# Kernel tuning notes

Measured on AMD Instinct MI355X. Metric: run time of the kernel, lower is better.

## Reference

```python
import jax, jax.numpy as jnp
import numpy as np

H = 128  # per-direction hidden size; bidirectional output = 256


def sru_layer(x, W, b):
    """One bidirectional SRU layer (use_selu=1).
    x: (L, B, n_in); W: (n_in, 2H*k); b: (4H,) = [f-bias(2H), r-bias(2H)].
    """
    L, B, n_in = x.shape
    k = W.shape[1] // (2 * H)  # 4 if n_in != 2H else 3
    U = (x @ W).reshape(L, B, 2, H, k)  # (L,B,dir,H,k)
    bf = b[: 2 * H].reshape(2, H)
    br = b[2 * H :].reshape(2, H)
    # highway input: learned projection (k==4) or the input itself split per direction
    xp = U[..., 3] if k == 4 else x.reshape(L, B, 2, H)
    # time-reverse the backward direction so a single scan serves both
    Us = jnp.stack([U[:, :, 0, :, :3], U[::-1, :, 1, :, :3]], axis=2)  # (L,B,2,H,3)
    xps = jnp.stack([xp[:, :, 0], xp[::-1, :, 1]], axis=2)  # (L,B,2,H)

    def step(c, t):
        u, xpt = t
        xt = u[..., 0]
        f = jax.nn.sigmoid(u[..., 1] + bf)
        r = jax.nn.sigmoid(u[..., 2] + br)
        c = f * c + (1.0 - f) * xt
        h = r * jax.nn.selu(c) + (1.0 - r) * xpt
        return c, h

    c0 = jnp.zeros((B, 2, H), x.dtype)
    _, hs = jax.lax.scan(step, c0, (Us, xps))  # hs: (L,B,2,H)
    # un-reverse backward direction, concat directions -> (L,B,2H)
    return jnp.concatenate([hs[:, :, 0], hs[::-1, :, 1]], axis=-1)


def setup_inputs() -> dict:
    key = jax.random.key(0)
    ks = jax.random.split(key, 6)
    L, B, D = 1024, 64, 128
    inp = {
        "input": jax.random.normal(ks[0], (L, B, D), jnp.float32),
        "W0": jax.random.normal(ks[1], (D, 4 * 2 * H), jnp.float32) / np.sqrt(D),
        "b0": jnp.zeros((4 * H,), jnp.float32),
        "gamma": jnp.ones((2 * H,), jnp.float32),
        "beta": jnp.zeros((2 * H,), jnp.float32),
    }
    for i, kk in zip((1, 2, 3), ks[2:5]):
        inp[f"W{i}"] = jax.random.normal(kk, (2 * H, 3 * 2 * H), jnp.float32) / np.sqrt(2 * H)
        inp[f"b{i}"] = jnp.zeros((4 * H,), jnp.float32)
    return inp


def reference(input, W0, b0, W1, b1, W2, b2, W3, b3, gamma, beta):
    x = sru_layer(input, W0, b0)
    x = sru_layer(x, W1, b1)
    x = sru_layer(x, W2, b2)
    x = sru_layer(x, W3, b3)  # (L,B,256)
    # permute(1,2,0) + avg_pool1d over full length + squeeze == mean over time
    feats = jnp.mean(x, axis=0)  # (B,256)
    mu = jnp.mean(feats, axis=-1, keepdims=True)
    var = jnp.mean(jnp.square(feats - mu), axis=-1, keepdims=True)
    return (feats - mu) / jnp.sqrt(var + 1e-5) * gamma + beta
```

## Files before the change

kernel.cpp:

```cpp
#include <hip/hip_runtime.h>
#include <math.h>

#define HID 128
#define LSEQ 1024
#define NB 64
#define SUB 32
#define NQG (LSEQ / SUB)
#define NCH 16384

typedef __attribute__((ext_vector_type(4))) float f32x4;
typedef __attribute__((ext_vector_type(8))) short bf16x8;
typedef __attribute__((ext_vector_type(8))) unsigned short u16x8;
typedef __attribute__((ext_vector_type(4))) unsigned short u16x4;

#define VMCNT0() asm volatile("s_waitcnt vmcnt(0)" ::: "memory")
#define VMCNT8() asm volatile("s_waitcnt vmcnt(8)" ::: "memory")
#define LGKMCNT0() asm volatile("s_waitcnt lgkmcnt(0)" ::: "memory")

__device__ __forceinline__ unsigned short f2bf(float x) {
    union { float f; unsigned int u; } a; a.f = x;
    unsigned int r = a.u + 0x7FFFu + ((a.u >> 16) & 1u);
    return (unsigned short)(r >> 16);
}
__device__ __forceinline__ float bf2f(unsigned short h) {
    union { float f; unsigned int u; } a; a.u = ((unsigned int)h) << 16;
    return a.f;
}
__device__ __forceinline__ float sigmoidf_(float x) { return 1.0f / (1.0f + __expf(-x)); }
__device__ __forceinline__ float seluf_(float x) {
    const float sc = 1.0507009873554805f, al = 1.6732632423543772f;
    return x > 0.0f ? sc * x : sc * al * (__expf(x) - 1.0f);
}

__device__ __forceinline__ void gload16(const unsigned short* g, unsigned short* l) {
    __builtin_amdgcn_global_load_lds(
        (const __attribute__((address_space(1))) unsigned int*)g,
        (__attribute__((address_space(3))) unsigned int*)l, 16, 0, 0);
}

__global__ __launch_bounds__(256) void conv_wt(const float* __restrict__ W,
                                               unsigned short* __restrict__ Wt,
                                               int K, int N, int kw) {
    int idx = blockIdx.x * 256 + threadIdx.x;
    if (idx >= K * N) return;
    int k = idx / N, n = idx - k * N;
    const int dir = n / (128 * kw);
    const int rem = n - dir * 128 * kw;
    const int h = rem / kw, j = rem - h * kw;
    const int np = dir * 128 * kw + j * 128 + h;
    Wt[(size_t)np * K + k] = f2bf(W[idx]);
}

__global__ __launch_bounds__(256) void conv_in(const float* __restrict__ in,
                                               unsigned short* __restrict__ outp,
                                               int n4) {
    int idx = blockIdx.x * 256 + threadIdx.x;
    if (idx >= n4) return;
    const float4 v = *reinterpret_cast<const float4*>(in + (size_t)idx * 4);
    u16x4 w;
    w[0] = f2bf(v.x); w[1] = f2bf(v.y); w[2] = f2bf(v.z); w[3] = f2bf(v.w);
    *(u16x4*)(outp + (size_t)idx * 4) = w;
}

template <int K, int NC>
__global__ __launch_bounds__(256) void gemm_v4(const unsigned short* __restrict__ A,
                                               const unsigned short* __restrict__ Bt,
                                               unsigned short* __restrict__ C) {
    constexpr int NN = NC / 128;
    constexpr int NT = K / 64;
    __shared__ __align__(16) unsigned short smA[2][128 * 64];
    __shared__ __align__(16) unsigned short smB[2][128 * 64];

    const int bid = blockIdx.x;
    const int mi = bid & 7;
    const int tt = bid >> 3;
    const int n = tt % NN;
    const int mg = tt / NN;
    const int m0 = (mg * 8 + mi) * 128;
    const int n0 = n * 128;

    const int tid = threadIdx.x;
    const int r = tid >> 3, c8 = tid & 7;
    const int swz = (c8 * 8) ^ ((r & 7) * 8);

    const int lane = tid & 63;
    const int wid = tid >> 6;
    const int wr = wid >> 1, wc = wid & 1;
    const int rlo = lane & 15, g = lane >> 4;

    f32x4 acc[4][4] = {};

    const unsigned short* gA = A + (size_t)m0 * K + swz;
    const unsigned short* gB = Bt + (size_t)n0 * K + swz;

#pragma unroll
    for (int i = 0; i < 4; ++i) {
        gload16(gA + (size_t)(r + 32 * i) * K, &smA[0][i * 2048 + tid * 8]);
        gload16(gB + (size_t)(r + 32 * i) * K, &smB[0][i * 2048 + tid * 8]);
    }
    if (NT > 1) {
#pragma unroll
        for (int i = 0; i < 4; ++i) {
            gload16(gA + (size_t)(r + 32 * i) * K + 64, &smA[1][i * 2048 + tid * 8]);
            gload16(gB + (size_t)(r + 32 * i) * K + 64, &smB[1][i * 2048 + tid * 8]);
        }
        VMCNT8();
    } else {
        VMCNT0();
    }
    __builtin_amdgcn_sched_barrier(0);
    __builtin_amdgcn_s_barrier();

#pragma unroll
    for (int t = 0; t < NT; ++t) {
        const int cur = t & 1;
        bf16x8 af[2][4], bff[2][4];
#pragma unroll
        for (int kk = 0; kk < 2; ++kk) {
            const int ke = kk * 32 + g * 8;
#pragma unroll
            for (int m = 0; m < 4; ++m) {
                const int row = wr * 64 + m * 16 + rlo;
                af[kk][m] = *(const bf16x8*)(&smA[cur][row * 64 + (ke ^ ((row & 7) * 8))]);
            }
#pragma unroll
            for (int nn2 = 0; nn2 < 4; ++nn2) {
                const int row = wc * 64 + nn2 * 16 + rlo;
                bff[kk][nn2] = *(const bf16x8*)(&smB[cur][row * 64 + (ke ^ ((row & 7) * 8))]);
            }
        }
        LGKMCNT0();
        __builtin_amdgcn_sched_barrier(0);
        __builtin_amdgcn_s_barrier();
        if (t + 2 < NT) {
            const int k0 = (t + 2) * 64;
#pragma unroll
            for (int i = 0; i < 4; ++i) {
                gload16(gA + (size_t)(r + 32 * i) * K + k0, &smA[cur][i * 2048 + tid * 8]);
                gload16(gB + (size_t)(r + 32 * i) * K + k0, &smB[cur][i * 2048 + tid * 8]);
            }
        }
        __builtin_amdgcn_sched_barrier(0);
#pragma unroll
        for (int kk = 0; kk < 2; ++kk)
#pragma unroll
            for (int m = 0; m < 4; ++m)
#pragma unroll
                for (int nn2 = 0; nn2 < 4; ++nn2)
                    acc[m][nn2] = __builtin_amdgcn_mfma_f32_16x16x32_bf16(
                        af[kk][m], bff[kk][nn2], acc[m][nn2], 0, 0, 0);
        if (t + 1 < NT) {
            if (t + 2 < NT) { VMCNT8(); } else { VMCNT0(); }
            __builtin_amdgcn_sched_barrier(0);
            __builtin_amdgcn_s_barrier();
        }
    }
    __syncthreads();

    unsigned short* ep = &smA[0][0];
#pragma unroll
    for (int m = 0; m < 4; ++m)
#pragma unroll
        for (int nn2 = 0; nn2 < 4; ++nn2) {
            const int col = wc * 64 + nn2 * 16 + rlo;
#pragma unroll
            for (int j = 0; j < 4; ++j) {
                const int row = wr * 64 + m * 16 + g * 4 + j;
                const int chunk = (col >> 3) ^ (row & 15);
                ep[row * 128 + chunk * 8 + (col & 7)] = f2bf(acc[m][nn2][j]);
            }
        }
    __syncthreads();
    {
        const int rr = tid >> 1;
        const int cb = (tid & 1) * 8;
#pragma unroll
        for (int k2 = 0; k2 < 8; ++k2) {
            const int c = cb + k2;
            const int pc = c ^ (rr & 15);
            const u16x8 v = *(const u16x8*)(&ep[rr * 128 + pc * 8]);
            *(u16x8*)(&C[(size_t)(m0 + rr) * NC + n0 + c * 8]) = v;
        }
    }
}


template <int NC>
__global__ __launch_bounds__(256) void scanA(const unsigned short* __restrict__ U,
                                             const float* __restrict__ bias,
                                             float* __restrict__ aArr,
                                             float* __restrict__ bArr,
                                             int dirbase, int dbstride,
                                             int chmask, int chshift, int T) {
    const int gid = blockIdx.x * 256 + threadIdx.x;
    const int fc = gid & chmask;
    const int q = gid >> chshift;
    const int dir = dirbase + (fc >> 13);
    const int b = (fc >> 7) & 63, h = fc & 127;
    const int dbase = (fc >> 13) * dbstride;
    const float bfb = bias[dir * HID + h];

    float aa = 1.0f, cc = 0.0f;
#pragma unroll 4
    for (int i = 0; i < SUB; ++i) {
        const int s = q * SUB + i;
        const int t = dir ? (T - 1 - s) : s;
        const size_t m = (size_t)t * NB + b;
        const float u0 = bf2f(U[m * NC + dbase + h]);
        const float u1 = bf2f(U[m * NC + dbase + 128 + h]);
        const float f = sigmoidf_(u1 + bfb);
        cc = f * cc + (1.0f - f) * u0;
        aa *= f;
    }
    const int fcg = dir * 8192 + (fc & 8191);
    aArr[(size_t)q * NCH + fcg] = aa;
    bArr[(size_t)q * NCH + fcg] = cc;
}

template <int Q>
__global__ __launch_bounds__(256) void scanB(const float* __restrict__ aArr,
                                             const float* __restrict__ bArr,
                                             float* __restrict__ cin,
                                             float* __restrict__ carry,
                                             int init, int fcg0) {
    const int fcg = fcg0 + blockIdx.x * 256 + threadIdx.x;
    float a[Q], bb[Q];
#pragma unroll
    for (int q = 0; q < Q; ++q) {
        a[q]  = aArr[(size_t)q * NCH + fcg];
        bb[q] = bArr[(size_t)q * NCH + fcg];
    }
    float c = init ? 0.0f : carry[fcg];
#pragma unroll
    for (int q = 0; q < Q; ++q) {
        cin[(size_t)q * NCH + fcg] = c;
        c = a[q] * c + bb[q];
    }
    carry[fcg] = c;
}

template <int NC, bool XP_FROM_U, bool ACC>
__global__ __launch_bounds__(256) void scanC(const unsigned short* __restrict__ U,
                                             const unsigned short* __restrict__ Xprev,
                                             const float* __restrict__ bias,
                                             const float* __restrict__ cin,
                                             unsigned short* __restrict__ Xout,
                                             float* __restrict__ part,
                                             int dirbase, int dbstride,
                                             int chmask, int chshift,
                                             int T, int t0, int qg0) {
    const int gid = blockIdx.x * 256 + threadIdx.x;
    const int fc = gid & chmask;
    const int q = gid >> chshift;
    const int dir = dirbase + (fc >> 13);
    const int b = (fc >> 7) & 63, h = fc & 127;
    const int dbase = (fc >> 13) * dbstride;
    const float bfb = bias[dir * HID + h];
    const float brb = bias[2 * HID + dir * HID + h];
    const int fcg = dir * 8192 + (fc & 8191);

    float c = cin[(size_t)q * NCH + fcg];
    float psum = 0.0f;
#pragma unroll 4
    for (int i = 0; i < SUB; ++i) {
        const int s = q * SUB + i;
        const int t = dir ? (T - 1 - s) : s;
        const size_t m = (size_t)t * NB + b;
        const size_t xrow = ((size_t)(t0 + t) * NB + b) * (2 * HID) + dir * HID + h;
        const float u0 = bf2f(U[m * NC + dbase + h]);
        const float u1 = bf2f(U[m * NC + dbase + 128 + h]);
        const float u2 = bf2f(U[m * NC + dbase + 256 + h]);
        float xp;
        if constexpr (XP_FROM_U) xp = bf2f(U[m * NC + dbase + 384 + h]);
        else                     xp = bf2f(Xprev[xrow]);
        const float f = sigmoidf_(u1 + bfb);
        const float r = sigmoidf_(u2 + brb);
        c = f * c + (1.0f - f) * u0;
        const float ho = r * seluf_(c) + (1.0f - r) * xp;
        if constexpr (ACC) psum += ho;
        else               Xout[xrow] = f2bf(ho);
    }
    if constexpr (ACC)
        part[(size_t)(qg0 + q) * (NB * 256) + b * 256 + dir * HID + h] = psum;
}

__global__ __launch_bounds__(256) void pool2(const float* __restrict__ part,
                                             const float* __restrict__ gamma,
                                             const float* __restrict__ beta,
                                             float* __restrict__ out) {
    const int b = blockIdx.x, chn = threadIdx.x;
    float s = 0.0f;
#pragma unroll
    for (int i = 0; i < NQG; ++i) s += part[(size_t)i * (NB * 256) + b * 256 + chn];
    const float feat = s * (1.0f / LSEQ);
    __shared__ float red[256];
    red[chn] = feat; __syncthreads();
    for (int off = 128; off > 0; off >>= 1) { if (chn < off) red[chn] += red[chn + off]; __syncthreads(); }
    const float mu = red[0] * (1.0f / 256.0f);
    __syncthreads();
    const float d = feat - mu;
    red[chn] = d * d; __syncthreads();
    for (int off = 128; off > 0; off >>= 1) { if (chn < off) red[chn] += red[chn + off]; __syncthreads(); }
    const float var = red[0] * (1.0f / 256.0f);
    out[b * 256 + chn] = d * rsqrtf(var + 1e-5f) * gamma[chn] + beta[chn];
}

extern "C" void kernel_launch(void* const* d_in, const int* in_sizes, int n_in,
                              void* d_out, int out_size, void* d_ws, size_t ws_size,
                              hipStream_t stream) {
    const float* input = (const float*)d_in[0];
    const float* gamma = (const float*)d_in[3];
    const float* beta  = (const float*)d_in[4];
    const float* Wl[4] = { (const float*)d_in[1], (const float*)d_in[5],
                           (const float*)d_in[7], (const float*)d_in[9] };
    const float* bl[4] = { (const float*)d_in[2], (const float*)d_in[6],
                           (const float*)d_in[8], (const float*)d_in[10] };
    float* out = (float*)d_out;

    char* base = (char*)d_ws;
    size_t off = 0;
    auto alloc = [&](size_t bytes) { size_t o = off; off = (off + bytes + 255) & ~(size_t)255; return o; };

    unsigned short* Wt[4];
    Wt[0] = (unsigned short*)(base + alloc((size_t)1024 * 128 * 2));
    for (int i = 1; i < 4; ++i) Wt[i] = (unsigned short*)(base + alloc((size_t)768 * 256 * 2));
    unsigned short* Xa = (unsigned short*)(base + alloc((size_t)LSEQ * NB * 256 * 2));
    unsigned short* Xb = (unsigned short*)(base + alloc((size_t)LSEQ * NB * 256 * 2));
    unsigned short* Xc = (unsigned short*)(base + alloc((size_t)LSEQ * NB * 128 * 2));
    float* carry = (float*)(base + alloc((size_t)NCH * 4));
    float* aArr  = (float*)(base + alloc((size_t)32 * NCH * 4));
    float* bArr  = (float*)(base + alloc((size_t)32 * NCH * 4));
    float* cinArr= (float*)(base + alloc((size_t)32 * NCH * 4));
    float* part  = (float*)(base + alloc((size_t)NQG * NB * 256 * 4));
    if (ws_size < off + (1u << 21)) return;
    const size_t uavail = ws_size - off;
    unsigned short* U = (unsigned short*)(base + off);

    conv_in<<<(LSEQ * NB * 128 / 4 + 255) / 256, 256, 0, stream>>>(input, Xc, LSEQ * NB * 128 / 4);
    conv_wt<<<(128 * 1024 + 255) / 256, 256, 0, stream>>>(Wl[0], Wt[0], 128, 1024, 4);
    for (int i = 1; i < 4; ++i)
        conv_wt<<<(256 * 768 + 255) / 256, 256, 0, stream>>>(Wl[i], Wt[i], 256, 768, 3);

    const unsigned short* Xin[4] = { Xc, Xa, Xb, Xa };
    unsigned short* Xout[4] = { Xa, Xb, Xa, nullptr };

    if (uavail >= (size_t)LSEQ * NB * 1024 * 2) {
        const int T = LSEQ, Q = T / SUB;
        const int nm = T * NB / 128;
        const dim3 sgrid(NCH * Q / 256);
        for (int layer = 0; layer < 4; ++layer) {
            const int kw = (layer == 0) ? 4 : 3;
            const int dbstride = 128 * kw;
            if (layer == 0)
                gemm_v4<128, 1024><<<dim3(nm * 8), 256, 0, stream>>>(Xin[0], Wt[0], U);
            else
                gemm_v4<256, 768><<<dim3(nm * 6), 256, 0, stream>>>(Xin[layer], Wt[layer], U);
            if (layer == 0)
                scanA<1024><<<sgrid, 256, 0, stream>>>(U, bl[0], aArr, bArr, 0, dbstride,
                                                       NCH - 1, 14, T);
            else
                scanA<768><<<sgrid, 256, 0, stream>>>(U, bl[layer], aArr, bArr, 0, dbstride,
                                                      NCH - 1, 14, T);
            scanB<32><<<NCH / 256, 256, 0, stream>>>(aArr, bArr, cinArr, carry, 1, 0);
            if (layer == 0)
                scanC<1024, true, false><<<sgrid, 256, 0, stream>>>(
                    U, nullptr, bl[0], cinArr, Xout[0], nullptr, 0, dbstride, NCH - 1, 14, T, 0, 0);
            else if (layer < 3)
                scanC<768, false, false><<<sgrid, 256, 0, stream>>>(
                    U, Xin[layer], bl[layer], cinArr, Xout[layer], nullptr, 0, dbstride,
                    NCH - 1, 14, T, 0, 0);
            else
                scanC<768, false, true><<<sgrid, 256, 0, stream>>>(
                    U, Xin[3], bl[3], cinArr, nullptr, part, 0, dbstride, NCH - 1, 14, T, 0, 0);
        }
    } else {
        int T = 0;
        for (int t = 512; t >= SUB; t >>= 1)
            if ((size_t)t * NB * 512 * 2 <= uavail) { T = t; break; }
        if (T == 0) return;
        const int C = LSEQ / T, Q = T / SUB;
        const int nm = T * NB / 128;
        const dim3 sgrid(8192 * Q / 256);
        for (int layer = 0; layer < 4; ++layer) {
            const int kw = (layer == 0) ? 4 : 3;
            const int K = (layer == 0) ? 128 : 256;
            const int Nc = 128 * kw;
            for (int dir = 0; dir < 2; ++dir) {
                const unsigned short* Bts = Wt[layer] + (size_t)dir * Nc * K;
                for (int cc = 0; cc < C; ++cc) {
                    const int ci = dir ? (C - 1 - cc) : cc;
                    const unsigned short* Ap = Xin[layer] + (size_t)ci * T * NB * K;
                    if (layer == 0)
                        gemm_v4<128, 512><<<dim3(nm * 4), 256, 0, stream>>>(Ap, Bts, U);
                    else
                        gemm_v4<256, 384><<<dim3(nm * 3), 256, 0, stream>>>(Ap, Bts, U);
                    if (layer == 0)
                        scanA<512><<<sgrid, 256, 0, stream>>>(U, bl[0], aArr, bArr, dir, 0,
                                                              8191, 13, T);
                    else
                        scanA<384><<<sgrid, 256, 0, stream>>>(U, bl[layer], aArr, bArr, dir, 0,
                                                              8191, 13, T);
                    if (Q == 16)
                        scanB<16><<<32, 256, 0, stream>>>(aArr, bArr, cinArr, carry,
                                                          cc == 0 ? 1 : 0, dir * 8192);
                    else
                        scanB<32><<<32, 256, 0, stream>>>(aArr, bArr, cinArr, carry,
                                                          cc == 0 ? 1 : 0, dir * 8192);
                    if (layer == 0)
                        scanC<512, true, false><<<sgrid, 256, 0, stream>>>(
                            U, nullptr, bl[0], cinArr, Xout[0], nullptr, dir, 0,
                            8191, 13, T, ci * T, ci * Q);
                    else if (layer < 3)
                        scanC<384, false, false><<<sgrid, 256, 0, stream>>>(
                            U, Xin[layer], bl[layer], cinArr, Xout[layer], nullptr, dir, 0,
                            8191, 13, T, ci * T, ci * Q);
                    else
                        scanC<384, false, true><<<sgrid, 256, 0, stream>>>(
                            U, Xin[3], bl[3], cinArr, nullptr, part, dir, 0,
                            8191, 13, T, ci * T, ci * Q);
                }
            }
        }
    }
    pool2<<<NB, 256, 0, stream>>>(part, gamma, beta, out);
}
```

Baseline: 489.2 us.

## Restructure GEMM to keep B tile resident and stream A per-wave

Replaces the 128x128 double-buffered GEMM with one where each block holds the full-K B tile (128 columns) in LDS and loops over four 128-row M tiles. Each wave streams its own 32-row A slices through a 4-slot ring with 3-deep prefetch, so the loop needs no block-wide barriers. The LDS epilogue is dropped in favour of direct u16x4 global stores. The aim is to reuse B across more rows and cut synchronisation, at the cost of narrower, less coalesced output stores, more LDS per block, and fewer blocks in the grid.

```diff
diff --git a/kernel.cpp b/kernel.cpp
--- a/kernel.cpp
+++ b/kernel.cpp
@@ -13,9 +13,10 @@
 typedef __attribute__((ext_vector_type(8))) unsigned short u16x8;
 typedef __attribute__((ext_vector_type(4))) unsigned short u16x4;
 
-#define VMCNT0() asm volatile("s_waitcnt vmcnt(0)" ::: "memory")
-#define VMCNT8() asm volatile("s_waitcnt vmcnt(8)" ::: "memory")
-#define LGKMCNT0() asm volatile("s_waitcnt lgkmcnt(0)" ::: "memory")
+template <int N>
+__device__ __forceinline__ void vmcntN() {
+    asm volatile("s_waitcnt vmcnt(%0)" :: "n"(N) : "memory");
+}
 
 __device__ __forceinline__ unsigned short f2bf(float x) {
     union { float f; unsigned int u; } a; a.f = x;
@@ -63,127 +64,104 @@
 }
 
 template <int K, int NC>
-__global__ __launch_bounds__(256) void gemm_v4(const unsigned short* __restrict__ A,
+__global__ __launch_bounds__(256) void gemm_v5(const unsigned short* __restrict__ A,
                                                const unsigned short* __restrict__ Bt,
                                                unsigned short* __restrict__ C) {
     constexpr int NN = NC / 128;
     constexpr int NT = K / 64;
-    __shared__ __align__(16) unsigned short smA[2][128 * 64];
-    __shared__ __align__(16) unsigned short smB[2][128 * 64];
+    constexpr int NSTEP = 4 * NT;
+    __shared__ __align__(16) unsigned short smB[NT * 128 * 64];
+    __shared__ __align__(16) unsigned short smA[4][4][2048];
 
     const int bid = blockIdx.x;
     const int mi = bid & 7;
     const int tt = bid >> 3;
     const int n = tt % NN;
-    const int mg = tt / NN;
-    const int m0 = (mg * 8 + mi) * 128;
+    const int mg = (tt / NN) * 8 + mi;
+    const int mb = mg * 512;
     const int n0 = n * 128;
 
     const int tid = threadIdx.x;
-    const int r = tid >> 3, c8 = tid & 7;
-    const int swz = (c8 * 8) ^ ((r & 7) * 8);
-
-    const int lane = tid & 63;
-    const int wid = tid >> 6;
-    const int wr = wid >> 1, wc = wid & 1;
-    const int rlo = lane & 15, g = lane >> 4;
-
-    f32x4 acc[4][4] = {};
-
-    const unsigned short* gA = A + (size_t)m0 * K + swz;
-    const unsigned short* gB = Bt + (size_t)n0 * K + swz;
-
-#pragma unroll
-    for (int i = 0; i < 4; ++i) {
-        gload16(gA + (size_t)(r + 32 * i) * K, &smA[0][i * 2048 + tid * 8]);
-        gload16(gB + (size_t)(r + 32 * i) * K, &smB[0][i * 2048 + tid * 8]);
-    }
-    if (NT > 1) {
-#pragma unroll
-        for (int i = 0; i < 4; ++i) {
-            gload16(gA + (size_t)(r + 32 * i) * K + 64, &smA[1][i * 2048 + tid * 8]);
-            gload16(gB + (size_t)(r + 32 * i) * K + 64, &smB[1][i * 2048 + tid * 8]);
-        }
-        VMCNT8();
-    } else {
-        VMCNT0();
-    }
+    const int w = tid >> 6, l = tid & 63;
+    const int rlo = l & 15, g = l >> 4;
+    const int kx = (l & 7) ^ (l >> 3);
+    const int kswz = (rlo & 7) * 8;
+
+#pragma unroll
+    for (int kt = 0; kt < NT; ++kt)
+#pragma unroll
+        for (int rd = 0; rd < 4; ++rd) {
+            const int col = rd * 32 + (tid >> 3);
+            const int kxb = (tid & 7) ^ ((tid >> 3) & 7);
+            gload16(Bt + (size_t)(n0 + col) * K + kt * 64 + kxb * 8,
+                    &smB[kt * 8192 + rd * 2048 + tid * 8]);
+        }
+
+    auto stageA = [&](int s2) {
+        const int mt2 = s2 / NT, kt2 = s2 % NT, sl = s2 & 3;
+        const int rowb = mb + mt2 * 128 + w * 32;
+#pragma unroll
+        for (int i = 0; i < 4; ++i)
+            gload16(A + (size_t)(rowb + i * 8 + (l >> 3)) * K + kt2 * 64 + kx * 8,
+                    &smA[w][sl][i * 512 + l * 8]);
+    };
+
+    stageA(0); stageA(1); stageA(2);
+    vmcntN<8>();
     __builtin_amdgcn_sched_barrier(0);
     __builtin_amdgcn_s_barrier();
-
-#pragma unroll
-    for (int t = 0; t < NT; ++t) {
-        const int cur = t & 1;
-        bf16x8 af[2][4], bff[2][4];
+    __builtin_amdgcn_sched_barrier(0);
+
+    f32x4 acc[2][8];
+#pragma unroll
+    for (int s = 0; s < NSTEP; ++s) {
+        const int mt = s / NT, kt = s % NT, slot = s & 3;
+        if (kt == 0) {
+#pragma unroll
+            for (int mf = 0; mf < 2; ++mf)
+#pragma unroll
+                for (int nf = 0; nf < 8; ++nf) acc[mf][nf] = (f32x4){0.f, 0.f, 0.f, 0.f};
+        }
+        if (s + 3 < NSTEP) { stageA(s + 3); vmcntN<12>(); }
+        else if (s + 3 == NSTEP) vmcntN<8>();
+        else if (s + 2 == NSTEP) vmcntN<4>();
+        else                     vmcntN<0>();
+        __builtin_amdgcn_sched_barrier(0);
+
 #pragma unroll
         for (int kk = 0; kk < 2; ++kk) {
-            const int ke = kk * 32 + g * 8;
-#pragma unroll
-            for (int m = 0; m < 4; ++m) {
-                const int row = wr * 64 + m * 16 + rlo;
-                af[kk][m] = *(const bf16x8*)(&smA[cur][row * 64 + (ke ^ ((row & 7) * 8))]);
+            const int koff = (kk * 32 + g * 8) ^ kswz;
+            bf16x8 af[2], bff[8];
+#pragma unroll
+            for (int mf = 0; mf < 2; ++mf)
+                af[mf] = *(const bf16x8*)(&smA[w][slot][(mf * 16 + rlo) * 64 + koff]);
+#pragma unroll
+            for (int nf = 0; nf < 8; ++nf)
+                bff[nf] = *(const bf16x8*)(&smB[kt * 8192 + (nf * 16 + rlo) * 64 + koff]);
+#pragma unroll
+            for (int mf = 0; mf < 2; ++mf)
+#pragma unroll
+                for (int nf = 0; nf < 8; ++nf)
+                    acc[mf][nf] = __builtin_amdgcn_mfma_f32_16x16x32_bf16(
+                        bff[nf], af[mf], acc[mf][nf], 0, 0, 0);
+        }
+
+        if (kt == NT - 1) {
+            const int rowb = mb + mt * 128 + w * 32;
+#pragma unroll
+            for (int mf = 0; mf < 2; ++mf) {
+                const size_t rbase = (size_t)(rowb + mf * 16 + rlo) * NC + n0 + g * 4;
+#pragma unroll
+                for (int nf = 0; nf < 8; ++nf) {
+                    u16x4 v;
+                    v[0] = f2bf(acc[mf][nf][0]); v[1] = f2bf(acc[mf][nf][1]);
+                    v[2] = f2bf(acc[mf][nf][2]); v[3] = f2bf(acc[mf][nf][3]);
+                    *(u16x4*)(&C[rbase + nf * 16]) = v;
+                }
             }
-#pragma unroll
-            for (int nn2 = 0; nn2 < 4; ++nn2) {
-                const int row = wc * 64 + nn2 * 16 + rlo;
-                bff[kk][nn2] = *(const bf16x8*)(&smB[cur][row * 64 + (ke ^ ((row & 7) * 8))]);
-            }
-        }
-        LGKMCNT0();
-        __builtin_amdgcn_sched_barrier(0);
-        __builtin_amdgcn_s_barrier();
-        if (t + 2 < NT) {
-            const int k0 = (t + 2) * 64;
-#pragma unroll
-            for (int i = 0; i < 4; ++i) {
-                gload16(gA + (size_t)(r + 32 * i) * K + k0, &smA[cur][i * 2048 + tid * 8]);
-                gload16(gB + (size_t)(r + 32 * i) * K + k0, &smB[cur][i * 2048 + tid * 8]);
-            }
-        }
-        __builtin_amdgcn_sched_barrier(0);
-#pragma unroll
-        for (int kk = 0; kk < 2; ++kk)
-#pragma unroll
-            for (int m = 0; m < 4; ++m)
-#pragma unroll
-                for (int nn2 = 0; nn2 < 4; ++nn2)
-                    acc[m][nn2] = __builtin_amdgcn_mfma_f32_16x16x32_bf16(
-                        af[kk][m], bff[kk][nn2], acc[m][nn2], 0, 0, 0);
-        if (t + 1 < NT) {
-            if (t + 2 < NT) { VMCNT8(); } else { VMCNT0(); }
-            __builtin_amdgcn_sched_barrier(0);
-            __builtin_amdgcn_s_barrier();
-        }
-    }
-    __syncthreads();
-
-    unsigned short* ep = &smA[0][0];
-#pragma unroll
-    for (int m = 0; m < 4; ++m)
-#pragma unroll
-        for (int nn2 = 0; nn2 < 4; ++nn2) {
-            const int col = wc * 64 + nn2 * 16 + rlo;
-#pragma unroll
-            for (int j = 0; j < 4; ++j) {
-                const int row = wr * 64 + m * 16 + g * 4 + j;
-                const int chunk = (col >> 3) ^ (row & 15);
-                ep[row * 128 + chunk * 8 + (col & 7)] = f2bf(acc[m][nn2][j]);
-            }
-        }
-    __syncthreads();
-    {
-        const int rr = tid >> 1;
-        const int cb = (tid & 1) * 8;
-#pragma unroll
-        for (int k2 = 0; k2 < 8; ++k2) {
-            const int c = cb + k2;
-            const int pc = c ^ (rr & 15);
-            const u16x8 v = *(const u16x8*)(&ep[rr * 128 + pc * 8]);
-            *(u16x8*)(&C[(size_t)(m0 + rr) * NC + n0 + c * 8]) = v;
-        }
-    }
-}
-
+        }
+    }
+}
 
 template <int NC>
 __global__ __launch_bounds__(256) void scanA(const unsigned short* __restrict__ U,
@@ -346,15 +324,14 @@
 
     if (uavail >= (size_t)LSEQ * NB * 1024 * 2) {
         const int T = LSEQ, Q = T / SUB;
-        const int nm = T * NB / 128;
         const dim3 sgrid(NCH * Q / 256);
         for (int layer = 0; layer < 4; ++layer) {
             const int kw = (layer == 0) ? 4 : 3;
             const int dbstride = 128 * kw;
             if (layer == 0)
-                gemm_v4<128, 1024><<<dim3(nm * 8), 256, 0, stream>>>(Xin[0], Wt[0], U);
+                gemm_v5<128, 1024><<<dim3(8 * 128), 256, 0, stream>>>(Xin[0], Wt[0], U);
             else
-                gemm_v4<256, 768><<<dim3(nm * 6), 256, 0, stream>>>(Xin[layer], Wt[layer], U);
+                gemm_v5<256, 768><<<dim3(6 * 128), 256, 0, stream>>>(Xin[layer], Wt[layer], U);
             if (layer == 0)
                 scanA<1024><<<sgrid, 256, 0, stream>>>(U, bl[0], aArr, bArr, 0, dbstride,
                                                        NCH - 1, 14, T);
@@ -375,11 +352,11 @@
         }
     } else {
         int T = 0;
-        for (int t = 512; t >= SUB; t >>= 1)
+        for (int t = 512; t >= 64; t >>= 1)
             if ((size_t)t * NB * 512 * 2 <= uavail) { T = t; break; }
         if (T == 0) return;
         const int C = LSEQ / T, Q = T / SUB;
-        const int nm = T * NB / 128;
+        const int nmg = T * NB / 512;
         const dim3 sgrid(8192 * Q / 256);
         for (int layer = 0; layer < 4; ++layer) {
             const int kw = (layer == 0) ? 4 : 3;
@@ -391,9 +368,9 @@
                     const int ci = dir ? (C - 1 - cc) : cc;
                     const unsigned short* Ap = Xin[layer] + (size_t)ci * T * NB * K;
                     if (layer == 0)
-                        gemm_v4<128, 512><<<dim3(nm * 4), 256, 0, stream>>>(Ap, Bts, U);
+                        gemm_v5<128, 512><<<dim3(4 * nmg), 256, 0, stream>>>(Ap, Bts, U);
                     else
-                        gemm_v4<256, 384><<<dim3(nm * 3), 256, 0, stream>>>(Ap, Bts, U);
+                        gemm_v5<256, 384><<<dim3(3 * nmg), 256, 0, stream>>>(Ap, Bts, U);
                     if (layer == 0)
                         scanA<512><<<sgrid, 256, 0, stream>>>(U, bl[0], aArr, bArr, dir, 0,
                                                               8191, 13, T);
```

Result: faster. 404.3 us (-17.3%).
